# Optimization experiments

Hardware: AMD Instinct MI355X
Metric: run time of the kernel (lower is better)

## Reference

```python
import math
import jax, jax.numpy as jnp
import numpy as np

D_SCALES = 4  # MSGAD d parameter


def calc_thetas(d):
    # Numeric replication of calculate_theta2 (beta-wavelet polynomial coeffs).
    # p_i(x) = (x/2)^i (1 - x/2)^(d-i) / (2 * Beta(i+1, d+1-i)); keep the d
    # lowest-order coefficients (constant .. x^{d-1}), matching the original.
    thetas = []
    for i in range(d):
        beta = math.factorial(i) * math.factorial(d - i) / math.factorial(d + 1)
        p = (np.poly1d([0.5, 0.0]) ** i) * (np.poly1d([-0.5, 1.0]) ** (d - i)) / (2.0 * beta)
        c = p.coeffs  # highest degree first, length d+1
        thetas.append([float(c[d - j]) for j in range(d)])
    return thetas

THETAS = calc_thetas(D_SCALES)


def setup_inputs() -> dict:
    key = jax.random.key(0)
    k1, k2, k3, k4 = jax.random.split(key, 4)
    N, E, IN, H = 8192, 262144, 256, 128
    in_feat = jax.random.normal(k1, (N, IN), dtype=jnp.float32)
    W = jax.random.normal(k2, (IN, H), dtype=jnp.float32) * 0.05
    b = jnp.zeros((H,), dtype=jnp.float32)
    src = jax.random.randint(k3, (E,), 0, N, dtype=jnp.int32)
    dst = jax.random.randint(k4, (E,), 0, N, dtype=jnp.int32)
    return {"in_feat": in_feat, "W": W, "b": b, "src": src, "dst": dst}


def reference(in_feat, W, b, src, dst):
    N = in_feat.shape[0]
    # Linear + LeakyReLU encoder
    h = jax.nn.leaky_relu(in_feat @ W + b, negative_slope=0.01)
    # dgl.add_self_loop
    loop = jnp.arange(N, dtype=src.dtype)
    s = jnp.concatenate([src, loop])
    d_ = jnp.concatenate([dst, loop])
    # out-degrees (with self loops), D^{-1/2} with clamp(min=1)
    deg = jax.ops.segment_sum(jnp.ones_like(s, dtype=jnp.float32), s, num_segments=N)
    dinv = jnp.maximum(deg, 1.0) ** -0.5  # [N]
    dinv = dinv[:, None]
    outs = []
    for theta in THETAS:
        feat = h
        acc = theta[0] * h
        for k in range(1, len(theta)):
            # unnormalized Laplacian: feat - D^{-1/2} A D^{-1/2} feat
            agg = jax.ops.segment_sum((feat * dinv)[s], d_, num_segments=N)
            feat = feat - agg * dinv
            acc = acc + theta[k] * feat
        outs.append(jnp.einsum('nd,md->nm', acc, acc))  # x @ x.T reconstruction
    return jnp.stack(outs)  # [d, N, N]
```

## Files before the change

### kernel.cpp

```cpp
#include <hip/hip_runtime.h>
#include <hip/hip_bf16.h>

#define N_NODES 8192
#define IN_DIM  256
#define H_DIM   128
#define N_EDGES 262144

typedef __attribute__((ext_vector_type(8))) short bf16x8;
typedef __attribute__((ext_vector_type(4))) float f32x4;

__global__ void hist_kernel(const int* __restrict__ src, const int* __restrict__ dst,
                            int* __restrict__ degc, int* __restrict__ dstc) {
    int e = blockIdx.x * 256 + threadIdx.x;
    if (e < N_EDGES) {
        atomicAdd(&degc[src[e]], 1);
        atomicAdd(&dstc[dst[e]], 1);
    }
}

__global__ void dinv_kernel(const int* __restrict__ degc, float* __restrict__ dinv) {
    int n = blockIdx.x * 256 + threadIdx.x;
    if (n < N_NODES) dinv[n] = 1.0f / sqrtf((float)(degc[n] + 1));
}

__global__ void scan_kernel(const int* __restrict__ cnt, int* __restrict__ rowptr,
                            int* __restrict__ cursor) {
    __shared__ int partial[256];
    int tid = threadIdx.x;
    const int chunk = N_NODES / 256;
    int base = tid * chunk;
    int s = 0;
    for (int i = 0; i < chunk; ++i) s += cnt[base + i];
    partial[tid] = s;
    __syncthreads();
    if (tid == 0) {
        int run = 0;
        for (int i = 0; i < 256; ++i) { int v = partial[i]; partial[i] = run; run += v; }
        rowptr[N_NODES] = run;
    }
    __syncthreads();
    int run = partial[tid];
    for (int i = 0; i < chunk; ++i) {
        rowptr[base + i] = run;
        cursor[base + i] = run;
        run += cnt[base + i];
    }
}

__global__ void fill_kernel(const int* __restrict__ src, const int* __restrict__ dst,
                            int* __restrict__ cursor, int* __restrict__ colidx) {
    int e = blockIdx.x * 256 + threadIdx.x;
    if (e < N_EDGES) {
        int p = atomicAdd(&cursor[dst[e]], 1);
        colidx[p] = src[e];
    }
}

__global__ __launch_bounds__(256) void gemm_h_kernel(const float* __restrict__ X,
                                                     const float* __restrict__ W,
                                                     const float* __restrict__ b,
                                                     const float* __restrict__ dinv,
                                                     float* __restrict__ F0,
                                                     float* __restrict__ tmp0) {
    __shared__ float xs[8][IN_DIM];
    int tid  = threadIdx.x;
    int col  = tid & 127;
    int half = tid >> 7;
    int row0 = blockIdx.x * 8;
    for (int i = tid; i < 8 * IN_DIM; i += 256)
        xs[i >> 8][i & 255] = X[(size_t)(row0 + (i >> 8)) * IN_DIM + (i & 255)];
    __syncthreads();
    float s0 = 0.f, s1 = 0.f, s2 = 0.f, s3 = 0.f;
    int r0 = half * 4;
    for (int k = 0; k < IN_DIM; ++k) {
        float wv = W[k * H_DIM + col];
        s0 += xs[r0 + 0][k] * wv;
        s1 += xs[r0 + 1][k] * wv;
        s2 += xs[r0 + 2][k] * wv;
        s3 += xs[r0 + 3][k] * wv;
    }
    float bb = b[col];
    float sv[4] = {s0, s1, s2, s3};
    for (int r = 0; r < 4; ++r) {
        int row = row0 + r0 + r;
        float v = sv[r] + bb;
        v = v > 0.f ? v : 0.01f * v;
        F0[(size_t)row * H_DIM + col]   = v;
        tmp0[(size_t)row * H_DIM + col] = v * dinv[row];
    }
}

__global__ __launch_bounds__(128) void prop_kernel(const float* __restrict__ Fin,
                                                   const float* __restrict__ tmpin,
                                                   float* __restrict__ Fout,
                                                   float* __restrict__ tmpout,
                                                   const float* __restrict__ dinv,
                                                   const int* __restrict__ rowptr,
                                                   const int* __restrict__ colidx) {
    int n = blockIdx.x;
    int j = threadIdx.x;
    float dv  = dinv[n];
    float fs  = Fin[(size_t)n * H_DIM + j];
    float sum = tmpin[(size_t)n * H_DIM + j];
    int beg = rowptr[n], end = rowptr[n + 1];
    for (int e = beg; e < end; ++e) {
        int srcn = colidx[e];
        sum += tmpin[(size_t)srcn * H_DIM + j];
    }
    float v = fs - sum * dv;
    Fout[(size_t)n * H_DIM + j]   = v;
    tmpout[(size_t)n * H_DIM + j] = v * dv;
}

__global__ __launch_bounds__(256) void acc_kernel(const float* __restrict__ F0,
                                                  const float* __restrict__ F1,
                                                  const float* __restrict__ F2,
                                                  const float* __restrict__ F3,
                                                  __hip_bfloat16* __restrict__ accb) {
    int i = blockIdx.x * 256 + threadIdx.x;
    const size_t NH = (size_t)N_NODES * H_DIM;
    float f0 = F0[i], f1 = F1[i], f2 = F2[i], f3 = F3[i];
    accb[0 * NH + i] = __float2bfloat16(2.5f * f0 - 5.0f * f1 + 3.75f * f2 - 1.25f * f3);
    accb[1 * NH + i] = __float2bfloat16(           5.0f * f1 - 7.5f  * f2 + 3.75f * f3);
    accb[2 * NH + i] = __float2bfloat16(                       3.75f * f2 - 3.75f * f3);
    accb[3 * NH + i] = __float2bfloat16(                                    1.25f * f3);
}

__global__ __launch_bounds__(256) void out_gemm_kernel(const __hip_bfloat16* __restrict__ accb,
                                                       float* __restrict__ out) {
    int t = blockIdx.z;
    const short* A = (const short*)accb + (size_t)t * N_NODES * H_DIM;
    int lane = threadIdx.x & 63;
    int w    = threadIdx.x >> 6;
    int wr = w >> 1, wc = w & 1;
    int brow = blockIdx.x * 128 + wr * 64;
    int bcol = blockIdx.y * 128 + wc * 64;
    int r16 = lane & 15;
    int kg  = lane >> 4;

    f32x4 c[4][4] = {};
    for (int kk = 0; kk < 4; ++kk) {
        int koff = kk * 32 + kg * 8;
        bf16x8 a[4], bfr[4];
#pragma unroll
        for (int m = 0; m < 4; ++m)
            a[m] = *(const bf16x8*)(A + (size_t)(brow + m * 16 + r16) * H_DIM + koff);
#pragma unroll
        for (int n = 0; n < 4; ++n)
            bfr[n] = *(const bf16x8*)(A + (size_t)(bcol + n * 16 + r16) * H_DIM + koff);
#pragma unroll
        for (int m = 0; m < 4; ++m)
#pragma unroll
            for (int n = 0; n < 4; ++n)
                c[m][n] = __builtin_amdgcn_mfma_f32_16x16x32_bf16(a[m], bfr[n], c[m][n], 0, 0, 0);
    }

    float* O = out + (size_t)t * N_NODES * N_NODES;
#pragma unroll
    for (int m = 0; m < 4; ++m)
#pragma unroll
        for (int n = 0; n < 4; ++n)
#pragma unroll
            for (int r = 0; r < 4; ++r) {
                int row = brow + m * 16 + kg * 4 + r;
                int col = bcol + n * 16 + r16;
                O[(size_t)row * N_NODES + col] = c[m][n][r];
            }
}

extern "C" void kernel_launch(void* const* d_in, const int* in_sizes, int n_in,
                              void* d_out, int out_size, void* d_ws, size_t ws_size,
                              hipStream_t stream) {
    const float* in_feat = (const float*)d_in[0];
    const float* W       = (const float*)d_in[1];
    const float* b       = (const float*)d_in[2];
    const int*   src     = (const int*)d_in[3];
    const int*   dst     = (const int*)d_in[4];
    float* out = (float*)d_out;

    char* ws = (char*)d_ws;
    const size_t NH4 = (size_t)N_NODES * H_DIM * sizeof(float);
    float* F0 = (float*)(ws + 0 * NH4);
    float* F1 = (float*)(ws + 1 * NH4);
    float* F2 = (float*)(ws + 2 * NH4);
    float* F3 = (float*)(ws + 3 * NH4);
    float* tA = (float*)(ws + 4 * NH4);
    float* tB = (float*)(ws + 5 * NH4);
    __hip_bfloat16* accb = (__hip_bfloat16*)(ws + 6 * NH4);
    char* p = ws + 8 * NH4;
    int*   degc   = (int*)p;   p += 32768;
    int*   dstc   = (int*)p;   p += 32768;
    float* dinv   = (float*)p; p += 32768;
    int*   rowptr = (int*)p;   p += 33792;
    int*   cursor = (int*)p;   p += 32768;
    int*   colidx = (int*)p;

    hipMemsetAsync(degc, 0, 32768, stream);
    hipMemsetAsync(dstc, 0, 32768, stream);

    hist_kernel<<<N_EDGES / 256, 256, 0, stream>>>(src, dst, degc, dstc);
    dinv_kernel<<<N_NODES / 256, 256, 0, stream>>>(degc, dinv);
    scan_kernel<<<1, 256, 0, stream>>>(dstc, rowptr, cursor);
    fill_kernel<<<N_EDGES / 256, 256, 0, stream>>>(src, dst, cursor, colidx);

    gemm_h_kernel<<<N_NODES / 8, 256, 0, stream>>>(in_feat, W, b, dinv, F0, tA);

    prop_kernel<<<N_NODES, 128, 0, stream>>>(F0, tA, F1, tB, dinv, rowptr, colidx);
    prop_kernel<<<N_NODES, 128, 0, stream>>>(F1, tB, F2, tA, dinv, rowptr, colidx);
    prop_kernel<<<N_NODES, 128, 0, stream>>>(F2, tA, F3, tB, dinv, rowptr, colidx);

    acc_kernel<<<(N_NODES * H_DIM) / 256, 256, 0, stream>>>(F0, F1, F2, F3, accb);

    dim3 g(N_NODES / 128, N_NODES / 128, 4);
    out_gemm_kernel<<<g, 256, 0, stream>>>(accb, out);
}
```

Measured before the change: 456.1 us.

## Move input GEMM to split-bf16 MFMA and vectorize scan, prop, acc, stores

Replaces the scalar FP32 encoder GEMM with an MFMA kernel. Inputs and weights are split into hi/lo bf16 parts, and three products are accumulated to approximate FP32 accuracy; this adds two conversion passes. The change also swaps the serial scan for a Hillis-Steele parallel scan and unrolls the neighbour gather by four. It vectorizes the accumulation kernel and writes output tiles as 16-byte vectors into the transposed position, relying on the symmetry of acc·accᵀ. The three-product bf16 split gives slightly lower precision than true FP32.

```diff
diff --git a/kernel.cpp b/kernel.cpp
--- a/kernel.cpp
+++ b/kernel.cpp
@@ -8,6 +8,16 @@
 
 typedef __attribute__((ext_vector_type(8))) short bf16x8;
 typedef __attribute__((ext_vector_type(4))) float f32x4;
+typedef __attribute__((ext_vector_type(4))) short s16x4;
+
+static __device__ inline short bf16_hi(float x) {
+    __hip_bfloat16 h = __float2bfloat16(x);
+    return *(short*)&h;
+}
+static __device__ inline float bf16_val(short s) {
+    __hip_bfloat16 h = *(__hip_bfloat16*)&s;
+    return __bfloat162float(h);
+}
 
 __global__ void hist_kernel(const int* __restrict__ src, const int* __restrict__ dst,
                             int* __restrict__ degc, int* __restrict__ dstc) {
@@ -25,21 +35,22 @@
 
 __global__ void scan_kernel(const int* __restrict__ cnt, int* __restrict__ rowptr,
                             int* __restrict__ cursor) {
-    __shared__ int partial[256];
+    __shared__ int buf[2][256];
     int tid = threadIdx.x;
     const int chunk = N_NODES / 256;
     int base = tid * chunk;
     int s = 0;
     for (int i = 0; i < chunk; ++i) s += cnt[base + i];
-    partial[tid] = s;
+    buf[0][tid] = s;
     __syncthreads();
-    if (tid == 0) {
-        int run = 0;
-        for (int i = 0; i < 256; ++i) { int v = partial[i]; partial[i] = run; run += v; }
-        rowptr[N_NODES] = run;
-    }
-    __syncthreads();
-    int run = partial[tid];
+    int pp = 0;
+    for (int off = 1; off < 256; off <<= 1) {
+        buf[pp ^ 1][tid] = buf[pp][tid] + (tid >= off ? buf[pp][tid - off] : 0);
+        pp ^= 1;
+        __syncthreads();
+    }
+    if (tid == 255) rowptr[N_NODES] = buf[pp][255];
+    int run = buf[pp][tid] - s;
     for (int i = 0; i < chunk; ++i) {
         rowptr[base + i] = run;
         cursor[base + i] = run;
@@ -56,38 +67,87 @@
     }
 }
 
-__global__ __launch_bounds__(256) void gemm_h_kernel(const float* __restrict__ X,
-                                                     const float* __restrict__ W,
-                                                     const float* __restrict__ b,
-                                                     const float* __restrict__ dinv,
-                                                     float* __restrict__ F0,
-                                                     float* __restrict__ tmp0) {
-    __shared__ float xs[8][IN_DIM];
-    int tid  = threadIdx.x;
-    int col  = tid & 127;
-    int half = tid >> 7;
-    int row0 = blockIdx.x * 8;
-    for (int i = tid; i < 8 * IN_DIM; i += 256)
-        xs[i >> 8][i & 255] = X[(size_t)(row0 + (i >> 8)) * IN_DIM + (i & 255)];
-    __syncthreads();
-    float s0 = 0.f, s1 = 0.f, s2 = 0.f, s3 = 0.f;
-    int r0 = half * 4;
-    for (int k = 0; k < IN_DIM; ++k) {
-        float wv = W[k * H_DIM + col];
-        s0 += xs[r0 + 0][k] * wv;
-        s1 += xs[r0 + 1][k] * wv;
-        s2 += xs[r0 + 2][k] * wv;
-        s3 += xs[r0 + 3][k] * wv;
-    }
-    float bb = b[col];
-    float sv[4] = {s0, s1, s2, s3};
-    for (int r = 0; r < 4; ++r) {
-        int row = row0 + r0 + r;
-        float v = sv[r] + bb;
-        v = v > 0.f ? v : 0.01f * v;
-        F0[(size_t)row * H_DIM + col]   = v;
-        tmp0[(size_t)row * H_DIM + col] = v * dinv[row];
-    }
+__global__ __launch_bounds__(256) void cvtX_kernel(const f32x4* __restrict__ X,
+                                                   s16x4* __restrict__ Xhi,
+                                                   s16x4* __restrict__ Xlo) {
+    int i = blockIdx.x * 256 + threadIdx.x;
+    f32x4 x = X[i];
+    s16x4 hi, lo;
+#pragma unroll
+    for (int j = 0; j < 4; ++j) {
+        short h = bf16_hi(x[j]);
+        hi[j] = h;
+        lo[j] = bf16_hi(x[j] - bf16_val(h));
+    }
+    Xhi[i] = hi;
+    Xlo[i] = lo;
+}
+
+__global__ __launch_bounds__(256) void cvtW_kernel(const float* __restrict__ W,
+                                                   short* __restrict__ Wthi,
+                                                   short* __restrict__ Wtlo) {
+    int t = blockIdx.x * 256 + threadIdx.x;
+    int k = t & 255, j = t >> 8;
+    float w = W[k * H_DIM + j];
+    short h = bf16_hi(w);
+    Wthi[t] = h;
+    Wtlo[t] = bf16_hi(w - bf16_val(h));
+}
+
+__global__ __launch_bounds__(256) void gemm_h_mfma(const short* __restrict__ Xhi,
+                                                   const short* __restrict__ Xlo,
+                                                   const short* __restrict__ Wthi,
+                                                   const short* __restrict__ Wtlo,
+                                                   const float* __restrict__ b,
+                                                   const float* __restrict__ dinv,
+                                                   float* __restrict__ F0,
+                                                   float* __restrict__ tmp0) {
+    int lane = threadIdx.x & 63;
+    int w    = threadIdx.x >> 6;
+    int wr = w >> 1, wc = w & 1;
+    int brow = blockIdx.x * 128 + wr * 64;
+    int bcol = wc * 64;
+    int r16 = lane & 15;
+    int kg  = lane >> 4;
+
+    f32x4 c[4][4] = {};
+    for (int kk = 0; kk < IN_DIM / 32; ++kk) {
+        int koff = kk * 32 + kg * 8;
+        bf16x8 ah[4], al[4], bh[4], bl[4];
+#pragma unroll
+        for (int m = 0; m < 4; ++m) {
+            size_t off = (size_t)(brow + m * 16 + r16) * IN_DIM + koff;
+            ah[m] = *(const bf16x8*)(Xhi + off);
+            al[m] = *(const bf16x8*)(Xlo + off);
+        }
+#pragma unroll
+        for (int n = 0; n < 4; ++n) {
+            size_t off = (size_t)(bcol + n * 16 + r16) * IN_DIM + koff;
+            bh[n] = *(const bf16x8*)(Wthi + off);
+            bl[n] = *(const bf16x8*)(Wtlo + off);
+        }
+#pragma unroll
+        for (int m = 0; m < 4; ++m)
+#pragma unroll
+            for (int n = 0; n < 4; ++n) {
+                c[m][n] = __builtin_amdgcn_mfma_f32_16x16x32_bf16(ah[m], bh[n], c[m][n], 0, 0, 0);
+                c[m][n] = __builtin_amdgcn_mfma_f32_16x16x32_bf16(ah[m], bl[n], c[m][n], 0, 0, 0);
+                c[m][n] = __builtin_amdgcn_mfma_f32_16x16x32_bf16(al[m], bh[n], c[m][n], 0, 0, 0);
+            }
+    }
+#pragma unroll
+    for (int m = 0; m < 4; ++m)
+#pragma unroll
+        for (int n = 0; n < 4; ++n)
+#pragma unroll
+            for (int r = 0; r < 4; ++r) {
+                int row = brow + m * 16 + kg * 4 + r;
+                int col = bcol + n * 16 + r16;
+                float v = c[m][n][r] + b[col];
+                v = v > 0.f ? v : 0.01f * v;
+                F0[(size_t)row * H_DIM + col]   = v;
+                tmp0[(size_t)row * H_DIM + col] = v * dinv[row];
+            }
 }
 
 __global__ __launch_bounds__(128) void prop_kernel(const float* __restrict__ Fin,
@@ -103,33 +163,50 @@
     float fs  = Fin[(size_t)n * H_DIM + j];
     float sum = tmpin[(size_t)n * H_DIM + j];
     int beg = rowptr[n], end = rowptr[n + 1];
-    for (int e = beg; e < end; ++e) {
-        int srcn = colidx[e];
-        sum += tmpin[(size_t)srcn * H_DIM + j];
-    }
+    int e = beg;
+    for (; e + 4 <= end; e += 4) {
+        int s0 = colidx[e], s1 = colidx[e + 1], s2 = colidx[e + 2], s3 = colidx[e + 3];
+        float v0 = tmpin[(size_t)s0 * H_DIM + j];
+        float v1 = tmpin[(size_t)s1 * H_DIM + j];
+        float v2 = tmpin[(size_t)s2 * H_DIM + j];
+        float v3 = tmpin[(size_t)s3 * H_DIM + j];
+        sum += v0 + v1 + v2 + v3;
+    }
+    for (; e < end; ++e)
+        sum += tmpin[(size_t)colidx[e] * H_DIM + j];
     float v = fs - sum * dv;
     Fout[(size_t)n * H_DIM + j]   = v;
     tmpout[(size_t)n * H_DIM + j] = v * dv;
 }
 
-__global__ __launch_bounds__(256) void acc_kernel(const float* __restrict__ F0,
-                                                  const float* __restrict__ F1,
-                                                  const float* __restrict__ F2,
-                                                  const float* __restrict__ F3,
-                                                  __hip_bfloat16* __restrict__ accb) {
+__global__ __launch_bounds__(256) void acc_kernel(const f32x4* __restrict__ F0,
+                                                  const f32x4* __restrict__ F1,
+                                                  const f32x4* __restrict__ F2,
+                                                  const f32x4* __restrict__ F3,
+                                                  s16x4* __restrict__ accb) {
     int i = blockIdx.x * 256 + threadIdx.x;
-    const size_t NH = (size_t)N_NODES * H_DIM;
-    float f0 = F0[i], f1 = F1[i], f2 = F2[i], f3 = F3[i];
-    accb[0 * NH + i] = __float2bfloat16(2.5f * f0 - 5.0f * f1 + 3.75f * f2 - 1.25f * f3);
-    accb[1 * NH + i] = __float2bfloat16(           5.0f * f1 - 7.5f  * f2 + 3.75f * f3);
-    accb[2 * NH + i] = __float2bfloat16(                       3.75f * f2 - 3.75f * f3);
-    accb[3 * NH + i] = __float2bfloat16(                                    1.25f * f3);
-}
-
-__global__ __launch_bounds__(256) void out_gemm_kernel(const __hip_bfloat16* __restrict__ accb,
+    const size_t NH4 = (size_t)N_NODES * H_DIM / 4;
+    f32x4 f0 = F0[i], f1 = F1[i], f2 = F2[i], f3 = F3[i];
+    f32x4 a0 = 2.5f * f0 - 5.0f * f1 + 3.75f * f2 - 1.25f * f3;
+    f32x4 a1 =           5.0f * f1 - 7.5f  * f2 + 3.75f * f3;
+    f32x4 a2 =                      3.75f * f2 - 3.75f * f3;
+    f32x4 a3 =                                   1.25f * f3;
+    s16x4 o0, o1, o2, o3;
+#pragma unroll
+    for (int j = 0; j < 4; ++j) {
+        o0[j] = bf16_hi(a0[j]); o1[j] = bf16_hi(a1[j]);
+        o2[j] = bf16_hi(a2[j]); o3[j] = bf16_hi(a3[j]);
+    }
+    accb[0 * NH4 + i] = o0;
+    accb[1 * NH4 + i] = o1;
+    accb[2 * NH4 + i] = o2;
+    accb[3 * NH4 + i] = o3;
+}
+
+__global__ __launch_bounds__(256) void out_gemm_kernel(const short* __restrict__ accb,
                                                        float* __restrict__ out) {
     int t = blockIdx.z;
-    const short* A = (const short*)accb + (size_t)t * N_NODES * H_DIM;
+    const short* A = accb + (size_t)t * N_NODES * H_DIM;
     int lane = threadIdx.x & 63;
     int w    = threadIdx.x >> 6;
     int wr = w >> 1, wc = w & 1;
@@ -159,13 +236,11 @@
 #pragma unroll
     for (int m = 0; m < 4; ++m)
 #pragma unroll
-        for (int n = 0; n < 4; ++n)
-#pragma unroll
-            for (int r = 0; r < 4; ++r) {
-                int row = brow + m * 16 + kg * 4 + r;
-                int col = bcol + n * 16 + r16;
-                O[(size_t)row * N_NODES + col] = c[m][n][r];
-            }
+        for (int n = 0; n < 4; ++n) {
+            int col  = bcol + n * 16 + r16;
+            int row0 = brow + m * 16 + kg * 4;
+            *(f32x4*)(O + (size_t)col * N_NODES + row0) = c[m][n];
+        }
 }
 
 extern "C" void kernel_launch(void* const* d_in, const int* in_sizes, int n_in,
@@ -186,14 +261,19 @@
     float* F3 = (float*)(ws + 3 * NH4);
     float* tA = (float*)(ws + 4 * NH4);
     float* tB = (float*)(ws + 5 * NH4);
-    __hip_bfloat16* accb = (__hip_bfloat16*)(ws + 6 * NH4);
+    char*  accb_region = ws + 6 * NH4;
+    short* accb = (short*)accb_region;
+    short* Xhi = (short*)accb_region;
+    short* Xlo = (short*)(accb_region + NH4);
     char* p = ws + 8 * NH4;
     int*   degc   = (int*)p;   p += 32768;
     int*   dstc   = (int*)p;   p += 32768;
     float* dinv   = (float*)p; p += 32768;
     int*   rowptr = (int*)p;   p += 33792;
     int*   cursor = (int*)p;   p += 32768;
-    int*   colidx = (int*)p;
+    int*   colidx = (int*)p;   p += (size_t)N_EDGES * 4;
+    short* Wthi   = (short*)p; p += 65536;
+    short* Wtlo   = (short*)p;
 
     hipMemsetAsync(degc, 0, 32768, stream);
     hipMemsetAsync(dstc, 0, 32768, stream);
@@ -203,13 +283,19 @@
     scan_kernel<<<1, 256, 0, stream>>>(dstc, rowptr, cursor);
     fill_kernel<<<N_EDGES / 256, 256, 0, stream>>>(src, dst, cursor, colidx);
 
-    gemm_h_kernel<<<N_NODES / 8, 256, 0, stream>>>(in_feat, W, b, dinv, F0, tA);
+    cvtX_kernel<<<(N_NODES * IN_DIM / 4) / 256, 256, 0, stream>>>((const f32x4*)in_feat,
+                                                                  (s16x4*)Xhi, (s16x4*)Xlo);
+    cvtW_kernel<<<(H_DIM * IN_DIM) / 256, 256, 0, stream>>>(W, Wthi, Wtlo);
+
+    gemm_h_mfma<<<N_NODES / 128, 256, 0, stream>>>(Xhi, Xlo, Wthi, Wtlo, b, dinv, F0, tA);
 
     prop_kernel<<<N_NODES, 128, 0, stream>>>(F0, tA, F1, tB, dinv, rowptr, colidx);
     prop_kernel<<<N_NODES, 128, 0, stream>>>(F1, tB, F2, tA, dinv, rowptr, colidx);
     prop_kernel<<<N_NODES, 128, 0, stream>>>(F2, tA, F3, tB, dinv, rowptr, colidx);
 
-    acc_kernel<<<(N_NODES * H_DIM) / 256, 256, 0, stream>>>(F0, F1, F2, F3, accb);
+    acc_kernel<<<(N_NODES * H_DIM / 4) / 256, 256, 0, stream>>>((const f32x4*)F0, (const f32x4*)F1,
+                                                                (const f32x4*)F2, (const f32x4*)F3,
+                                                                (s16x4*)accb);
 
     dim3 g(N_NODES / 128, N_NODES / 128, 4);
     out_gemm_kernel<<<g, 256, 0, stream>>>(accb, out);
```

Measured after the change: 445.5 us. 2.3% less time.
